# Optimization experiments

Hardware: AMD Instinct MI355X
Metric: run time of the kernel (lower is better)

Reference implementation:

```python
import jax, jax.numpy as jnp
import numpy as np

DIM = 768
NUM_HEADS = 12
HEAD_DIM = DIM // NUM_HEADS
SCALE = HEAD_DIM ** -0.5


def setup_inputs() -> dict:
    key = jax.random.key(0)
    k1, k2, k3, k4, k5 = jax.random.split(key, 5)
    B, N = 2, 2048
    x = jax.random.normal(k1, (B, N, DIM), dtype=jnp.float32)
    # nn.Linear weights stored as [out, in]; we keep them as [in, out] for jnp use.
    Wq = jax.random.normal(k2, (DIM, DIM), dtype=jnp.float32) * (DIM ** -0.5)
    Wkv = jax.random.normal(k3, (DIM, 2 * HEAD_DIM), dtype=jnp.float32) * (DIM ** -0.5)
    Wproj = jax.random.normal(k4, (DIM, DIM), dtype=jnp.float32) * (DIM ** -0.5)
    bproj = jax.random.normal(k5, (DIM,), dtype=jnp.float32) * 0.01
    return {"x": x, "Wq": Wq, "Wkv": Wkv, "Wproj": Wproj, "bproj": bproj, "num_layer": 0}


def reference(x, Wq, Wkv, Wproj, bproj, num_layer):
    B, N, C = x.shape
    H, D = NUM_HEADS, HEAD_DIM
    q = (x @ Wq).reshape(B, N, H, D).transpose(0, 2, 1, 3)        # [B,H,N,D]
    kv = (x @ Wkv).reshape(B, N, 2, D)
    k, v = kv[:, :, 0, :], kv[:, :, 1, :]                          # [B,N,D] shared across heads (MQA)
    attn = jnp.einsum('bhid,bjd->bhij', q, k) * SCALE              # [B,H,N,N]
    attn = jax.nn.softmax(attn, axis=-1)
    out = jnp.einsum('bhij,bjd->bhid', attn, v)                    # [B,H,N,D]
    out = out.transpose(0, 2, 1, 3).reshape(B, N, C)
    return out @ Wproj + bproj
```

## Files before the change

kernel.cpp:

```cpp
#include <hip/hip_runtime.h>

#define BATCH 2
#define SEQ   2048
#define DIMC  768
#define HEADS 12
#define HD    64
#define QSCALE 0.1803368801111204f

typedef short bf16x8 __attribute__((ext_vector_type(8)));
typedef float f32x4  __attribute__((ext_vector_type(4)));
typedef float f32x16 __attribute__((ext_vector_type(16)));

__device__ __forceinline__ unsigned short f2bf(float f) {
    union { float f; unsigned int u; } a; a.f = f;
    unsigned int r = a.u + 0x7fffu + ((a.u >> 16) & 1u);
    return (unsigned short)(r >> 16);
}
__device__ __forceinline__ unsigned int pack2bf(float lo, float hi) {
    union { float f; unsigned int u; } a, b; a.f = lo; b.f = hi;
    return __builtin_amdgcn_perm(b.u + 0x8000u, a.u + 0x8000u, 0x07060302);
}
__device__ __forceinline__ unsigned int cvtpk_bf16(float lo, float hi) {
    unsigned int r;
    asm("v_cvt_pk_bf16_f32 %0, %1, %2" : "=v"(r) : "v"(lo), "v"(hi));
    return r;
}
__device__ __forceinline__ float exp2f_fast(float x) { return __builtin_amdgcn_exp2f(x); }

__device__ __forceinline__ void gload16(const unsigned short* g, unsigned short* l) {
    __builtin_amdgcn_global_load_lds(
        (const __attribute__((address_space(1))) unsigned int*)g,
        (__attribute__((address_space(3))) unsigned int*)l, 16, 0, 0);
}

__global__ void prep(const float* __restrict__ Wq, const float* __restrict__ Wkv,
                     const float* __restrict__ Wproj, const float* __restrict__ x,
                     unsigned short* __restrict__ WqT, unsigned short* __restrict__ WkvT,
                     unsigned short* __restrict__ WprT, unsigned short* __restrict__ xb)
{
    const int bid = blockIdx.x, t = threadIdx.x;
    if (bid >= 1248) {
        const size_t base = (size_t)(bid - 1248) * 2048 + (size_t)t * 8;
        float4 v0 = *(const float4*)&x[base];
        float4 v1 = *(const float4*)&x[base + 4];
        uint4 o = { pack2bf(v0.x, v0.y), pack2bf(v0.z, v0.w),
                    pack2bf(v1.x, v1.y), pack2bf(v1.z, v1.w) };
        *(uint4*)&xb[base] = o;
        return;
    }
    __shared__ float sT[32][33];
    const float* W; unsigned short* WT; int N, tb;
    if (bid < 576)      { W = Wq;    WT = WqT;  N = DIMC;   tb = bid; }
    else if (bid < 672) { W = Wkv;   WT = WkvT; N = 2 * HD; tb = bid - 576; }
    else                { W = Wproj; WT = WprT; N = DIMC;   tb = bid - 672; }
    const int tilesN = N / 32;
    const int k0 = (tb / tilesN) * 32, n0 = (tb - (tb / tilesN) * tilesN) * 32;
    const int r = t >> 3, c4 = (t & 7) * 4;
    float4 v = *(const float4*)&W[(size_t)(k0 + r) * N + n0 + c4];
    sT[c4 + 0][r] = v.x; sT[c4 + 1][r] = v.y; sT[c4 + 2][r] = v.z; sT[c4 + 3][r] = v.w;
    __syncthreads();
    ushort4 o = { f2bf(sT[r][c4]), f2bf(sT[r][c4 + 1]), f2bf(sT[r][c4 + 2]), f2bf(sT[r][c4 + 3]) };
    *(ushort4*)&WT[(size_t)(n0 + r) * 768 + k0 + c4] = o;
}

template <int MODE>
__global__ __launch_bounds__(256)
void gemm64(const unsigned short* __restrict__ A, const unsigned short* __restrict__ BT,
            const float* __restrict__ bias, void* __restrict__ C0,
            unsigned short* __restrict__ Kout, unsigned short* __restrict__ VTout)
{
    __shared__ __align__(16) unsigned short sA[2][4096];
    __shared__ __align__(16) unsigned short sB[2][8192];
    const int t = threadIdx.x, lane = t & 63, w = t >> 6;
    const int bm = blockIdx.y * 64, bn = blockIdx.x * 128;
    const int wm = (w >> 1) * 32, wn = (w & 1) * 64;
    const int cr = lane >> 2, ck = (lane & 3) * 8;

    auto stage = [&](int kt, int bf) {
        #pragma unroll
        for (int q = 0; q < 2; ++q) {
            const int c = 2 * w + q, kc = c >> 2, rg = c & 3;
            gload16(&A[(size_t)(bm + rg * 16 + cr) * DIMC + kt * 64 + kc * 32 + ck],
                    &sA[bf][kc * 2048 + rg * 512]);
        }
        #pragma unroll
        for (int q = 0; q < 4; ++q) {
            const int c = 4 * w + q, kc = c >> 3, rg = c & 7;
            gload16(&BT[(size_t)(bn + rg * 16 + cr) * DIMC + kt * 64 + kc * 32 + ck],
                    &sB[bf][kc * 4096 + rg * 512]);
        }
    };

    const int fr = lane & 15, fk = (lane >> 4) * 8;
    f32x4 acc[2][4] = {};

    stage(0, 0);
    __syncthreads();
    for (int kt = 0; kt < DIMC / 64; ++kt) {
        const int buf = kt & 1;
        if (kt + 1 < DIMC / 64) stage(kt + 1, buf ^ 1);
        #pragma unroll
        for (int kc = 0; kc < 2; ++kc) {
            bf16x8 af[2], bq[4];
            #pragma unroll
            for (int i = 0; i < 2; ++i)
                af[i] = *(const bf16x8*)&sA[buf][kc * 2048 + (wm + i * 16 + fr) * 32 + fk];
            #pragma unroll
            for (int j = 0; j < 4; ++j)
                bq[j] = *(const bf16x8*)&sB[buf][kc * 4096 + (wn + j * 16 + fr) * 32 + fk];
            #pragma unroll
            for (int i = 0; i < 2; ++i)
                #pragma unroll
                for (int j = 0; j < 4; ++j)
                    acc[i][j] = __builtin_amdgcn_mfma_f32_16x16x32_bf16(af[i], bq[j], acc[i][j], 0, 0, 0);
        }
        __syncthreads();
    }

    const int cn = lane & 15, cm = (lane >> 4) * 4;
    #pragma unroll
    for (int j = 0; j < 4; ++j) {
        const int n = bn + wn + j * 16 + cn;
        #pragma unroll
        for (int i = 0; i < 2; ++i) {
            #pragma unroll
            for (int r = 0; r < 4; ++r) {
                const int m = bm + wm + i * 16 + cm + r;
                float val = acc[i][j][r];
                if (MODE == 0) {
                    if (n < DIMC) {
                        ((unsigned short*)C0)[(size_t)m * DIMC + n] = f2bf(val * QSCALE);
                    } else {
                        const int c2 = n - DIMC;
                        if (c2 < HD) Kout[(size_t)m * HD + c2] = f2bf(val);
                        else {
                            const int bbk = m >> 11, tok = m & (SEQ - 1);
                            VTout[(size_t)bbk * HD * SEQ + (size_t)(c2 - HD) * SEQ + tok] = f2bf(val);
                        }
                    }
                } else {
                    ((float*)C0)[(size_t)m * DIMC + n] = val + bias[n];
                }
            }
        }
    }
}

__global__ __launch_bounds__(256)
void flash_kernel(const unsigned short* __restrict__ Qw, const unsigned short* __restrict__ Kw,
                  const unsigned short* __restrict__ VTw, unsigned short* __restrict__ Ob)
{
    const int qblk = blockIdx.x, h = blockIdx.y, b = blockIdx.z;
    const int tid = threadIdx.x, w = tid >> 6, lane = tid & 63;
    const int l31 = lane & 31, hi = lane >> 5;
    const int kr = w >> 1, qc = w & 1;

    __shared__ __align__(16) unsigned short sK [2][64][72];
    __shared__ __align__(16) unsigned short sVT[2][64][72];
    __shared__ float sL[4][32];
    __shared__ float sLi[2][32];

    const size_t qrow = (size_t)(b * SEQ + qblk * 64 + qc * 32 + l31);
    bf16x8 qf[4];
    #pragma unroll
    for (int s = 0; s < 4; ++s)
        qf[s] = *(const bf16x8*)&Qw[qrow * DIMC + h * HD + s * 16 + hi * 8];

    f32x16 oacc0 = {}, oacc1 = {};
    float lsum = 0.0f;

    const int r_st = tid >> 2, c_st = (tid & 3) * 16;
    const unsigned short* Kp  = &Kw[(size_t)(b * SEQ + r_st) * HD + c_st];
    const unsigned short* VTp = &VTw[(size_t)b * HD * SEQ + (size_t)r_st * SEQ + c_st];

    bf16x8 kg0, kg1, vg0, vg1;
    auto loadKV = [&](int ti) {
        const unsigned short* ks = Kp + (size_t)ti * 64 * HD;
        const unsigned short* vs = VTp + ti * 64;
        kg0 = *(const bf16x8*)&ks[0]; kg1 = *(const bf16x8*)&ks[8];
        vg0 = *(const bf16x8*)&vs[0]; vg1 = *(const bf16x8*)&vs[8];
    };
    auto writeKV = [&](int bf) {
        *(bf16x8*)&sK[bf][r_st][c_st]      = kg0;
        *(bf16x8*)&sK[bf][r_st][c_st + 8]  = kg1;
        *(bf16x8*)&sVT[bf][r_st][c_st]     = vg0;
        *(bf16x8*)&sVT[bf][r_st][c_st + 8] = vg1;
    };

    loadKV(0); writeKV(0); loadKV(1);
    __syncthreads();

    for (int kt = 0; kt < SEQ / 64; ++kt) {
        const int buf = kt & 1;
        if (kt + 1 < SEQ / 64) {
            writeKV(buf ^ 1);
            loadKV(kt + 2 < SEQ / 64 ? kt + 2 : SEQ / 64 - 1);
        }

        f32x16 st = {};
        __builtin_amdgcn_s_setprio(1);
        #pragma unroll
        for (int s = 0; s < 4; ++s) {
            bf16x8 ka = *(const bf16x8*)&sK[buf][kr * 32 + l31][s * 16 + hi * 8];
            st = __builtin_amdgcn_mfma_f32_32x32x16_bf16(ka, qf[s], st, 0, 0, 0);
        }
        __builtin_amdgcn_s_setprio(0);

        uint2 pg[4];
        #pragma unroll
        for (int g = 0; g < 4; ++g) {
            float p0 = exp2f_fast(st[g * 4 + 0]);
            float p1 = exp2f_fast(st[g * 4 + 1]);
            float p2 = exp2f_fast(st[g * 4 + 2]);
            float p3 = exp2f_fast(st[g * 4 + 3]);
            lsum += (p0 + p1) + (p2 + p3);
            pg[g].x = cvtpk_bf16(p0, p1);
            pg[g].y = cvtpk_bf16(p2, p3);
        }

        #pragma unroll
        for (int s = 0; s < 2; ++s) {
            unsigned int ax = pg[2 * s].x, bx = pg[2 * s + 1].x;
            unsigned int ay = pg[2 * s].y, by = pg[2 * s + 1].y;
            asm("v_permlane32_swap_b32 %0, %1" : "+v"(ax), "+v"(bx));
            asm("v_permlane32_swap_b32 %0, %1" : "+v"(ay), "+v"(by));
            union { uint4 u4; bf16x8 v; } pa;
            pa.u4.x = ax;
            pa.u4.y = ay;
            pa.u4.z = bx;
            pa.u4.w = by;
            bf16x8 vb0 = *(const bf16x8*)&sVT[buf][l31][kr * 32 + s * 16 + hi * 8];
            bf16x8 vb1 = *(const bf16x8*)&sVT[buf][32 + l31][kr * 32 + s * 16 + hi * 8];
            __builtin_amdgcn_s_setprio(1);
            oacc0 = __builtin_amdgcn_mfma_f32_32x32x16_bf16(pa.v, vb0, oacc0, 0, 0, 0);
            oacc1 = __builtin_amdgcn_mfma_f32_32x32x16_bf16(pa.v, vb1, oacc1, 0, 0, 0);
            __builtin_amdgcn_s_setprio(0);
        }

        asm volatile("s_waitcnt lgkmcnt(0)" ::: "memory");
        __builtin_amdgcn_sched_barrier(0);
        __builtin_amdgcn_s_barrier();
    }

    lsum += __shfl_xor(lsum, 32);
    if (lane < 32) sL[w][l31] = lsum;

    float* scratch = (float*)&sK[0][0][0];
    {
        int rid = qc * 2 + (1 - kr);
        float* rg = scratch + rid * 1024;
        f32x16 give = kr ? oacc0 : oacc1;
        #pragma unroll
        for (int r = 0; r < 16; ++r) rg[r * 64 + lane] = give[r];
    }
    __syncthreads();

    f32x16 own = kr ? oacc1 : oacc0;
    {
        const float* rg = scratch + (qc * 2 + kr) * 1024;
        #pragma unroll
        for (int r = 0; r < 16; ++r) own[r] += rg[r * 64 + lane];
    }
    if (kr == 0 && lane < 32)
        sLi[qc][l31] = 1.0f / (sL[qc][l31] + sL[qc + 2][l31]);
    __syncthreads();

    #pragma unroll
    for (int r = 0; r < 16; ++r) {
        int rq = (r & 3) + 8 * (r >> 2) + 4 * hi;
        float iv = sLi[qc][rq];
        size_t row = (size_t)(b * SEQ + qblk * 64 + qc * 32 + rq);
        Ob[row * DIMC + h * HD + kr * 32 + l31] = f2bf(own[r] * iv);
    }
}

extern "C" void kernel_launch(void* const* d_in, const int* in_sizes, int n_in,
                              void* d_out, int out_size, void* d_ws, size_t ws_size,
                              hipStream_t stream)
{
    const float* x     = (const float*)d_in[0];
    const float* Wq    = (const float*)d_in[1];
    const float* Wkv   = (const float*)d_in[2];
    const float* Wproj = (const float*)d_in[3];
    const float* bproj = (const float*)d_in[4];

    const int M = BATCH * SEQ;
    unsigned short* WqT  = (unsigned short*)d_ws;
    unsigned short* WkvT = WqT  + DIMC * DIMC;
    unsigned short* WprT = WkvT + 2 * HD * DIMC;
    unsigned short* Qw   = WprT + DIMC * DIMC;
    unsigned short* Kw   = Qw   + (size_t)M * DIMC;
    unsigned short* VTw  = Kw   + (size_t)M * HD;
    unsigned short* Ob   = VTw  + (size_t)BATCH * HD * SEQ;
    unsigned short* xb   = Ob;

    prep<<<1248 + 1536, 256, 0, stream>>>(Wq, Wkv, Wproj, x, WqT, WkvT, WprT, xb);
    gemm64<0><<<dim3(7, M / 64), 256, 0, stream>>>(xb, WqT, nullptr, Qw, Kw, VTw);
    flash_kernel<<<dim3(SEQ / 64, HEADS, BATCH), 256, 0, stream>>>(Qw, Kw, VTw, Ob);
    gemm64<1><<<dim3(6, M / 64), 256, 0, stream>>>(Ob, WprT, bproj, d_out, nullptr, nullptr);
}
```

Baseline: 150.3 us.

## Load K tiles straight into MFMA registers, dropping the K shared-memory stage

The flash kernel now reads K fragments from global memory directly into registers in the MFMA operand layout, double-buffered across two register sets, with the key loop unrolled by two. Only V^T still goes through double-buffered LDS, and the final reduction scratch reuses the V^T buffer. This removes the K LDS writes and reads and frees shared memory. In exchange, waves sharing the same K rows issue redundant global loads, and register pressure rises. The launch bounds now also request four blocks per CU, which caps VGPRs and risks spills.

```diff
diff --git a/kernel.cpp b/kernel.cpp
--- a/kernel.cpp
+++ b/kernel.cpp
@@ -146,7 +146,7 @@
     }
 }
 
-__global__ __launch_bounds__(256)
+__global__ __launch_bounds__(256, 4)
 void flash_kernel(const unsigned short* __restrict__ Qw, const unsigned short* __restrict__ Kw,
                   const unsigned short* __restrict__ VTw, unsigned short* __restrict__ Ob)
 {
@@ -154,8 +154,8 @@
     const int tid = threadIdx.x, w = tid >> 6, lane = tid & 63;
     const int l31 = lane & 31, hi = lane >> 5;
     const int kr = w >> 1, qc = w & 1;
-
-    __shared__ __align__(16) unsigned short sK [2][64][72];
+    const int NT = SEQ / 64;
+
     __shared__ __align__(16) unsigned short sVT[2][64][72];
     __shared__ float sL[4][32];
     __shared__ float sLi[2][32];
@@ -170,40 +170,33 @@
     float lsum = 0.0f;
 
     const int r_st = tid >> 2, c_st = (tid & 3) * 16;
-    const unsigned short* Kp  = &Kw[(size_t)(b * SEQ + r_st) * HD + c_st];
     const unsigned short* VTp = &VTw[(size_t)b * HD * SEQ + (size_t)r_st * SEQ + c_st];
-
-    bf16x8 kg0, kg1, vg0, vg1;
-    auto loadKV = [&](int ti) {
-        const unsigned short* ks = Kp + (size_t)ti * 64 * HD;
+    bf16x8 vg0, vg1;
+    auto loadV = [&](int ti) {
         const unsigned short* vs = VTp + ti * 64;
-        kg0 = *(const bf16x8*)&ks[0]; kg1 = *(const bf16x8*)&ks[8];
         vg0 = *(const bf16x8*)&vs[0]; vg1 = *(const bf16x8*)&vs[8];
     };
-    auto writeKV = [&](int bf) {
-        *(bf16x8*)&sK[bf][r_st][c_st]      = kg0;
-        *(bf16x8*)&sK[bf][r_st][c_st + 8]  = kg1;
+    auto writeV = [&](int bf) {
         *(bf16x8*)&sVT[bf][r_st][c_st]     = vg0;
         *(bf16x8*)&sVT[bf][r_st][c_st + 8] = vg1;
     };
 
-    loadKV(0); writeKV(0); loadKV(1);
-    __syncthreads();
-
-    for (int kt = 0; kt < SEQ / 64; ++kt) {
-        const int buf = kt & 1;
-        if (kt + 1 < SEQ / 64) {
-            writeKV(buf ^ 1);
-            loadKV(kt + 2 < SEQ / 64 ? kt + 2 : SEQ / 64 - 1);
-        }
-
+    const unsigned short* Kbase = &Kw[((size_t)b * SEQ + kr * 32 + l31) * HD + hi * 8];
+    bf16x8 kA[4], kB[4];
+    auto loadK = [&](int ti, bf16x8* kf) {
+        const unsigned short* kp = Kbase + (size_t)ti * 64 * HD;
+        kf[0] = *(const bf16x8*)&kp[0];
+        kf[1] = *(const bf16x8*)&kp[16];
+        kf[2] = *(const bf16x8*)&kp[32];
+        kf[3] = *(const bf16x8*)&kp[48];
+    };
+
+    auto step = [&](const bf16x8* kf, int buf) {
         f32x16 st = {};
         __builtin_amdgcn_s_setprio(1);
         #pragma unroll
-        for (int s = 0; s < 4; ++s) {
-            bf16x8 ka = *(const bf16x8*)&sK[buf][kr * 32 + l31][s * 16 + hi * 8];
-            st = __builtin_amdgcn_mfma_f32_32x32x16_bf16(ka, qf[s], st, 0, 0, 0);
-        }
+        for (int s = 0; s < 4; ++s)
+            st = __builtin_amdgcn_mfma_f32_32x32x16_bf16(kf[s], qf[s], st, 0, 0, 0);
         __builtin_amdgcn_s_setprio(0);
 
         uint2 pg[4];
@@ -236,16 +229,33 @@
             oacc1 = __builtin_amdgcn_mfma_f32_32x32x16_bf16(pa.v, vb1, oacc1, 0, 0, 0);
             __builtin_amdgcn_s_setprio(0);
         }
-
+    };
+
+    auto bar = [&]() {
         asm volatile("s_waitcnt lgkmcnt(0)" ::: "memory");
         __builtin_amdgcn_sched_barrier(0);
         __builtin_amdgcn_s_barrier();
+    };
+
+    loadV(0); writeV(0); loadV(1);
+    loadK(0, kA); loadK(1, kB);
+    __syncthreads();
+
+    for (int kt = 0; kt < NT; kt += 2) {
+        if (kt + 1 < NT) { writeV(1); loadV(kt + 2 < NT ? kt + 2 : NT - 1); }
+        step(kA, 0);
+        if (kt + 2 < NT) loadK(kt + 2, kA);
+        bar();
+        if (kt + 2 < NT) { writeV(0); loadV(kt + 3 < NT ? kt + 3 : NT - 1); }
+        step(kB, 1);
+        if (kt + 3 < NT) loadK(kt + 3, kB);
+        bar();
     }
 
     lsum += __shfl_xor(lsum, 32);
     if (lane < 32) sL[w][l31] = lsum;
 
-    float* scratch = (float*)&sK[0][0][0];
+    float* scratch = (float*)&sVT[0][0][0];
     {
         int rid = qc * 2 + (1 - kr);
         float* rg = scratch + rid * 1024;
```

Result: slower. 206.1 us (+37.1%).
